# Kernel optimization log

Hardware: AMD Instinct MI355X
Metric: run time of the kernel (lower is better)

Reference implementation:

```python
import jax, jax.numpy as jnp
import numpy as np

B, CIN, COUT, H, W = 16, 64, 64, 128, 128
MH, MW = 32, 32  # retained Fourier modes


def setup_inputs() -> dict:
    key = jax.random.key(0)
    k1, k2, k3 = jax.random.split(key, 3)
    scale = 1.0 / (CIN * COUT)  # 'auto' scale in the torch module
    x = jax.random.normal(k1, (B, CIN, H, W), dtype=jnp.float32)
    # packed complex weight: dim0 = (real, imag), dim1 = corner (top=0, bottom=1)
    weight = scale * jax.random.normal(k2, (2, 2, CIN, COUT, MH, MW), dtype=jnp.float32)
    bias = scale * jax.random.normal(k3, (COUT, 1, 1), dtype=jnp.float32)
    return {"x": x, "weight": weight, "bias": bias, "super_res": 1}


def reference(x, weight, bias, super_res):
    b, ci, h, w = x.shape
    # rfft2 over the last two spatial dims (norm='backward' is default)
    xf = jnp.fft.rfft2(x.astype(jnp.float32), norm="backward")  # [b, ci, h, w//2+1] c64
    wc = (weight[0] + 1j * weight[1]).astype(jnp.complex64)  # [2, ci, co, mh, mw]
    # low-frequency corner contractions: bixy,ioxy->boxy
    top = jnp.einsum("bixy,ioxy->boxy", xf[:, :, :MH, :MW], wc[0])
    bot = jnp.einsum("bixy,ioxy->boxy", xf[:, :, h - MH:, :MW], wc[1])
    out_fft = jnp.zeros((b, COUT, h, w // 2 + 1), dtype=jnp.complex64)
    out_fft = out_fft.at[:, :, :MH, :MW:super_res].set(top)
    out_fft = out_fft.at[:, :, h - MH:, :MW:super_res].set(bot)
    out_size = (int(h * super_res), int(w * super_res))
    y = jnp.fft.irfft2(out_fft, s=out_size, norm="backward").astype(x.dtype)
    return y + bias  # bias [co,1,1] broadcasts over spatial dims
```

## Files before the change

kernel.cpp:

```cpp
#include <hip/hip_runtime.h>


__device__ __forceinline__ void build_tab(float* tabs) {
    int t = threadIdx.x;
    if (t < 128) {
        float ang = (float)t * 0.049087385212340517f;
        float s, c;
        sincosf(ang, &s, &c);
        tabs[t] = c;
        tabs[129 + t] = s;
    }
}

__global__ __launch_bounds__(256) void kAB(const float* __restrict__ x,
                                           float* __restrict__ XF) {
    __shared__ float tabs[258];
    __shared__ __align__(16) float smem[8704];
    build_tab(tabs);
    __syncthreads();
    int t = threadIdx.x;
    size_t bc = blockIdx.x;
    float* Twid = smem;
    float* xeo  = smem + 4096;
    #pragma unroll
    for (int i = 0; i < 16; ++i) {
        int e = t + i * 256;
        int w = e >> 6, q = e & 63, kx = q >> 1;
        int idx = (w * kx) & 127;
        Twid[e] = (q & 1) ? -tabs[129 + idx] : tabs[idx];
    }
    const float* xb = x + bc * 16384;
    int th = t & 31;
    int tq = t >> 5;
    int q0 = tq * 8;
    int wl4 = (t & 3) * 4;
    int hb  = t >> 2;
    float4 rlo0, rhi0, rlo1, rhi1;
    auto loadR = [&](int ph) {
        rlo0 = *(const float4*)(xb + hb * 128 + ph * 16 + wl4);
        rhi0 = *(const float4*)(xb + hb * 128 + ph * 16 + wl4 + 64);
        rlo1 = *(const float4*)(xb + (64 + hb) * 128 + ph * 16 + wl4);
        rhi1 = *(const float4*)(xb + (64 + hb) * 128 + ph * 16 + wl4 + 64);
    };
    auto writeR = [&]() {
        int h0 = hb, h1 = 64 + hb;
        *(float2*)(&xeo[(wl4+0)*260 + 2*h0]) = make_float2(rlo0.x+rhi0.x, rlo0.x-rhi0.x);
        *(float2*)(&xeo[(wl4+1)*260 + 2*h0]) = make_float2(rlo0.y+rhi0.y, rlo0.y-rhi0.y);
        *(float2*)(&xeo[(wl4+2)*260 + 2*h0]) = make_float2(rlo0.z+rhi0.z, rlo0.z-rhi0.z);
        *(float2*)(&xeo[(wl4+3)*260 + 2*h0]) = make_float2(rlo0.w+rhi0.w, rlo0.w-rhi0.w);
        *(float2*)(&xeo[(wl4+0)*260 + 2*h1]) = make_float2(rlo1.x+rhi1.x, rlo1.x-rhi1.x);
        *(float2*)(&xeo[(wl4+1)*260 + 2*h1]) = make_float2(rlo1.y+rhi1.y, rlo1.y-rhi1.y);
        *(float2*)(&xeo[(wl4+2)*260 + 2*h1]) = make_float2(rlo1.z+rhi1.z, rlo1.z-rhi1.z);
        *(float2*)(&xeo[(wl4+3)*260 + 2*h1]) = make_float2(rlo1.w+rhi1.w, rlo1.w-rhi1.w);
    };
    loadR(0);
    writeR();
    float4 acc[8];
    #pragma unroll
    for (int j = 0; j < 8; ++j) acc[j] = make_float4(0.f, 0.f, 0.f, 0.f);
    __syncthreads();
    for (int ph = 0; ph < 4; ++ph) {
        if (ph < 3) loadR(ph + 1);
        #pragma unroll 4
        for (int wl = 0; wl < 16; ++wl) {
            int w = ph * 16 + wl;
            const float* xr = &xeo[wl * 260 + 4 * th];
            float4 d0  = *(const float4*)(xr);
            float4 d1  = *(const float4*)(xr + 128);
            float4 tw0 = *(const float4*)(&Twid[w * 64 + q0]);
            float4 tw1 = *(const float4*)(&Twid[w * 64 + q0 + 4]);
            acc[0].x = fmaf(d0.x, tw0.x, acc[0].x); acc[0].y = fmaf(d0.x, tw0.y, acc[0].y);
            acc[0].z = fmaf(d0.y, tw0.z, acc[0].z); acc[0].w = fmaf(d0.y, tw0.w, acc[0].w);
            acc[1].x = fmaf(d0.x, tw1.x, acc[1].x); acc[1].y = fmaf(d0.x, tw1.y, acc[1].y);
            acc[1].z = fmaf(d0.y, tw1.z, acc[1].z); acc[1].w = fmaf(d0.y, tw1.w, acc[1].w);
            acc[2].x = fmaf(d0.z, tw0.x, acc[2].x); acc[2].y = fmaf(d0.z, tw0.y, acc[2].y);
            acc[2].z = fmaf(d0.w, tw0.z, acc[2].z); acc[2].w = fmaf(d0.w, tw0.w, acc[2].w);
            acc[3].x = fmaf(d0.z, tw1.x, acc[3].x); acc[3].y = fmaf(d0.z, tw1.y, acc[3].y);
            acc[3].z = fmaf(d0.w, tw1.z, acc[3].z); acc[3].w = fmaf(d0.w, tw1.w, acc[3].w);
            acc[4].x = fmaf(d1.x, tw0.x, acc[4].x); acc[4].y = fmaf(d1.x, tw0.y, acc[4].y);
            acc[4].z = fmaf(d1.y, tw0.z, acc[4].z); acc[4].w = fmaf(d1.y, tw0.w, acc[4].w);
            acc[5].x = fmaf(d1.x, tw1.x, acc[5].x); acc[5].y = fmaf(d1.x, tw1.y, acc[5].y);
            acc[5].z = fmaf(d1.y, tw1.z, acc[5].z); acc[5].w = fmaf(d1.y, tw1.w, acc[5].w);
            acc[6].x = fmaf(d1.z, tw0.x, acc[6].x); acc[6].y = fmaf(d1.z, tw0.y, acc[6].y);
            acc[6].z = fmaf(d1.w, tw0.z, acc[6].z); acc[6].w = fmaf(d1.w, tw0.w, acc[6].w);
            acc[7].x = fmaf(d1.z, tw1.x, acc[7].x); acc[7].y = fmaf(d1.z, tw1.y, acc[7].y);
            acc[7].z = fmaf(d1.w, tw1.z, acc[7].z); acc[7].w = fmaf(d1.w, tw1.w, acc[7].w);
        }
        __syncthreads();
        if (ph < 3) {
            writeR();
            __syncthreads();
        }
    }
    float* Af = smem;
    {
        int base = th * 68 + q0;
        *(float4*)(&Af[base])          = make_float4(acc[0].x+acc[4].x, acc[0].y+acc[4].y, acc[0].z+acc[4].z, acc[0].w+acc[4].w);
        *(float4*)(&Af[base + 4])      = make_float4(acc[1].x+acc[5].x, acc[1].y+acc[5].y, acc[1].z+acc[5].z, acc[1].w+acc[5].w);
        *(float4*)(&Af[2176 + base])   = make_float4(acc[0].x-acc[4].x, acc[0].y-acc[4].y, acc[0].z-acc[4].z, acc[0].w-acc[4].w);
        *(float4*)(&Af[2176 + base+4]) = make_float4(acc[1].x-acc[5].x, acc[1].y-acc[5].y, acc[1].z-acc[5].z, acc[1].w-acc[5].w);
        *(float4*)(&Af[4352 + base])   = make_float4(acc[2].x+acc[6].x, acc[2].y+acc[6].y, acc[2].z+acc[6].z, acc[2].w+acc[6].w);
        *(float4*)(&Af[4352 + base+4]) = make_float4(acc[3].x+acc[7].x, acc[3].y+acc[7].y, acc[3].z+acc[7].z, acc[3].w+acc[7].w);
        *(float4*)(&Af[6528 + base])   = make_float4(acc[2].x-acc[6].x, acc[2].y-acc[6].y, acc[2].z-acc[6].z, acc[2].w-acc[6].w);
        *(float4*)(&Af[6528 + base+4]) = make_float4(acc[3].x-acc[7].x, acc[3].y-acc[7].y, acc[3].z-acc[7].z, acc[3].w-acc[7].w);
    }
    __syncthreads();
    {
        int k = t & 31, kxg = t >> 5;
        int kx0 = kxg * 4;
        int sig = k & 1;
        const float* pe = Af + sig * 2176;
        const float* po = Af + 4352 + sig * 2176;
        int a2 = (2 * k) & 127;
        float ca = tabs[a2], sa = tabs[129 + a2];
        float ce = 1.f, se = 0.f;
        float co_ = tabs[k], so_ = tabs[129 + k];
        float4 P1 = {0,0,0,0}, P2 = {0,0,0,0}, P3 = {0,0,0,0}, P4 = {0,0,0,0};
        for (int m = 0; m < 32; ++m) {
            float4 ae01 = *(const float4*)(pe + m * 68 + 2 * kx0);
            float4 ae23 = *(const float4*)(pe + m * 68 + 2 * kx0 + 4);
            float4 ao01 = *(const float4*)(po + m * 68 + 2 * kx0);
            float4 ao23 = *(const float4*)(po + m * 68 + 2 * kx0 + 4);
            P1.x = fmaf(ae01.x, ce, P1.x); P1.x = fmaf(ao01.x, co_, P1.x);
            P2.x = fmaf(ae01.y, se, P2.x); P2.x = fmaf(ao01.y, so_, P2.x);
            P3.x = fmaf(ae01.y, ce, P3.x); P3.x = fmaf(ao01.y, co_, P3.x);
            P4.x = fmaf(ae01.x, se, P4.x); P4.x = fmaf(ao01.x, so_, P4.x);
            P1.y = fmaf(ae01.z, ce, P1.y); P1.y = fmaf(ao01.z, co_, P1.y);
            P2.y = fmaf(ae01.w, se, P2.y); P2.y = fmaf(ao01.w, so_, P2.y);
            P3.y = fmaf(ae01.w, ce, P3.y); P3.y = fmaf(ao01.w, co_, P3.y);
            P4.y = fmaf(ae01.z, se, P4.y); P4.y = fmaf(ao01.z, so_, P4.y);
            P1.z = fmaf(ae23.x, ce, P1.z); P1.z = fmaf(ao23.x, co_, P1.z);
            P2.z = fmaf(ae23.y, se, P2.z); P2.z = fmaf(ao23.y, so_, P2.z);
            P3.z = fmaf(ae23.y, ce, P3.z); P3.z = fmaf(ao23.y, co_, P3.z);
            P4.z = fmaf(ae23.x, se, P4.z); P4.z = fmaf(ao23.x, so_, P4.z);
            P1.w = fmaf(ae23.z, ce, P1.w); P1.w = fmaf(ao23.z, co_, P1.w);
            P2.w = fmaf(ae23.w, se, P2.w); P2.w = fmaf(ao23.w, so_, P2.w);
            P3.w = fmaf(ae23.w, ce, P3.w); P3.w = fmaf(ao23.w, co_, P3.w);
            P4.w = fmaf(ae23.z, se, P4.w); P4.w = fmaf(ao23.z, so_, P4.w);
            float t1 = se * sa, t2 = ce * sa;
            float cen = fmaf(ce, ca, -t1);
            float sen = fmaf(se, ca, t2);
            ce = cen; se = sen;
            float t3 = so_ * sa, t4 = co_ * sa;
            float con = fmaf(co_, ca, -t3);
            float son = fmaf(so_, ca, t4);
            co_ = con; so_ = son;
        }
        float* xfb = XF + bc * 4096;
        *(float4*)(xfb + (k * 32 + kx0) * 2) =
            make_float4(P1.x + P2.x, P3.x - P4.x, P1.y + P2.y, P3.y - P4.y);
        *(float4*)(xfb + (k * 32 + kx0) * 2 + 4) =
            make_float4(P1.z + P2.z, P3.z - P4.z, P1.w + P2.w, P3.w - P4.w);
        if (k) {
            *(float4*)(xfb + ((64 - k) * 32 + kx0) * 2) =
                make_float4(P1.x - P2.x, P3.x + P4.x, P1.y - P2.y, P3.y + P4.y);
            *(float4*)(xfb + ((64 - k) * 32 + kx0) * 2 + 4) =
                make_float4(P1.z - P2.z, P3.z + P4.z, P1.w - P2.w, P3.w + P4.w);
        }
        if (t < 32) {
            int kx = t;
            float re = 0.f, im = 0.f;
            #pragma unroll 8
            for (int m = 0; m < 32; ++m) {
                float2 aep = *(const float2*)(&Af[       m * 68 + 2 * kx]);
                float2 aop = *(const float2*)(&Af[4352 + m * 68 + 2 * kx]);
                float sg = (m & 1) ? -1.f : 1.f;
                re = fmaf(sg, aep.x - aop.y, re);
                im = fmaf(sg, aep.y + aop.x, im);
            }
            xfb[(32 * 32 + kx) * 2]     = re;
            xfb[(32 * 32 + kx) * 2 + 1] = im;
        }
    }
}

__global__ __launch_bounds__(256, 4) void kC(const float* __restrict__ XF,
                                             const float* __restrict__ Wgt,
                                             float* __restrict__ YF0,
                                             float* __restrict__ YF1) {
    __shared__ float2 Xs[2048];
    int t = threadIdx.x;
    int bid = blockIdx.x;
    int cih = bid & 1;
    int mxh = (bid >> 1) & 1;
    int cot = (bid >> 2) & 3;
    int my  = (bid >> 4) & 31;
    int c   = bid >> 9;
    int co0 = cot * 16;
    int slotbase = (c * 32 + my) * 32 + mxh * 16;
    int mx = t & 15;
    int co_l = t >> 4;
    int co = co0 + co_l;
    int ci0 = cih * 32;
    float2 acc[16];
    #pragma unroll
    for (int i = 0; i < 16; ++i) acc[i] = make_float2(0.f, 0.f);
    const float* wp = Wgt + (size_t)c * 4194304 + (size_t)my * 32 + mxh * 16 + mx
                          + ((size_t)(ci0 * 64) + co) * 1024;
    float2 rw0[8], rw1[8], rw2[8], rw3[8], rx[8];
    auto loadW = [&](int cc, float2* rw) {
        #pragma unroll
        for (int j = 0; j < 8; ++j) {
            size_t off = (size_t)(cc * 8 + j) * 65536;
            rw[j].x = wp[off];
            rw[j].y = wp[off + 8388608];
        }
    };
    auto loadX = [&](int cc) {
        #pragma unroll
        for (int s = 0; s < 8; ++s) {
            int e = t + s * 256;
            int emx = e & 15, eb = (e >> 4) & 15, eci = e >> 8;
            int ci = ci0 + cc * 8 + eci;
            rx[s] = *(const float2*)(XF + ((size_t)(eb * 64 + ci) * 2048 + slotbase + emx) * 2);
        }
    };
    auto writeX = [&]() {
        #pragma unroll
        for (int s = 0; s < 8; ++s) Xs[t + s * 256] = rx[s];
    };
#define KC_COMPUTE(RW)                                                       \
    {                                                                        \
        _Pragma("unroll")                                                    \
        for (int j = 0; j < 8; ++j) {                                        \
            float2 w = RW[j];                                                \
            _Pragma("unroll")                                                \
            for (int b = 0; b < 16; ++b) {                                   \
                float2 xv = Xs[(j * 16 + b) * 16 + mx];                      \
                acc[b].x = fmaf(xv.x, w.x, acc[b].x);                        \
                acc[b].x = fmaf(-xv.y, w.y, acc[b].x);                       \
                acc[b].y = fmaf(xv.x, w.y, acc[b].y);                        \
                acc[b].y = fmaf(xv.y, w.x, acc[b].y);                        \
            }                                                                \
        }                                                                    \
    }
    loadX(0);
    loadW(0, rw0); loadW(1, rw1); loadW(2, rw2);
    writeX();
    __syncthreads();
    loadX(1);
    loadW(3, rw3);
    KC_COMPUTE(rw0);
    __syncthreads();
    writeX(); __syncthreads();
    loadX(2);
    KC_COMPUTE(rw1);
    __syncthreads();
    writeX(); __syncthreads();
    loadX(3);
    KC_COMPUTE(rw2);
    __syncthreads();
    writeX(); __syncthreads();
    KC_COMPUTE(rw3);
#undef KC_COMPUTE
    float* YF = cih ? YF1 : YF0;
    #pragma unroll
    for (int b = 0; b < 16; ++b) {
        *(float2*)(YF + ((size_t)(b * 64 + co) * 2048 + slotbase + mx) * 2) = acc[b];
    }
}

__global__ __launch_bounds__(256) void kDE(const float* __restrict__ YF0,
                                           const float* __restrict__ YF1,
                                           const float* __restrict__ bias,
                                           float* __restrict__ out) {
    __shared__ float tabs[258];
    __shared__ __align__(16) float Ts[8192];
    __shared__ __align__(16) float U[8448];
    build_tab(tabs);
    __syncthreads();
    int t = threadIdx.x;
    size_t bo = blockIdx.x;
    const float inv = 6.103515625e-05f;
    #pragma unroll
    for (int i = 0; i < 32; ++i) {
        int e = t + i * 256;
        int q = e >> 7, w = e & 127;
        int k = q >> 1;
        int idx = (k * w) & 127;
        float val;
        if (q == 0)      val = inv;
        else if (q == 1) val = 0.f;
        else if (q & 1)  val = -2.f * inv * tabs[129 + idx];
        else             val =  2.f * inv * tabs[idx];
        Ts[e] = val;
    }
    float* Qs = U;
    float* Rs = U + 2112;
    const float* y0 = YF0 + bo * 4096;
    const float* y1 = YF1 + bo * 4096;
    for (int u = t; u < 528; u += 256) {
        int k = u >> 4, kxf = (u & 15) * 4;
        float4 a0 = *(const float4*)(y0 + k * 64 + kxf);
        float4 a1 = *(const float4*)(y1 + k * 64 + kxf);
        float4 a = make_float4(a0.x+a1.x, a0.y+a1.y, a0.z+a1.z, a0.w+a1.w);
        float4 Q, R;
        if (k == 0) { Q = a; R = make_float4(0.f, 0.f, 0.f, 0.f); }
        else if (k == 32) { Q = a; R = make_float4(-a.x, -a.y, -a.z, -a.w); }
        else {
            float4 b0 = *(const float4*)(y0 + (64 - k) * 64 + kxf);
            float4 b1 = *(const float4*)(y1 + (64 - k) * 64 + kxf);
            float4 bb = make_float4(b0.x+b1.x, b0.y+b1.y, b0.z+b1.z, b0.w+b1.w);
            Q = make_float4(a.x+bb.x, a.y+bb.y, a.z+bb.z, a.w+bb.w);
            R = make_float4(a.x-bb.x, a.y-bb.y, a.z-bb.z, a.w-bb.w);
        }
        *(float4*)(&Qs[k * 64 + kxf]) = Q;
        *(float4*)(&Rs[k * 64 + kxf]) = R;
    }
    __syncthreads();
    int hh = t >> 2;
    int kx0 = (t & 3) * 8;
    float4 Ee0 = {0,0,0,0}, Ee1 = {0,0,0,0}, Ee2 = {0,0,0,0}, Ee3 = {0,0,0,0};
    float4 Eo0 = {0,0,0,0}, Eo1 = {0,0,0,0}, Eo2 = {0,0,0,0}, Eo3 = {0,0,0,0};
    int idx = 0;
#define KD_BODY(E0, E1, E2, E3, kk)                                          \
    {                                                                        \
        float c = tabs[idx], s = tabs[129 + idx];                            \
        const float4* Qp = (const float4*)(&Qs[(kk) * 64 + kx0 * 2]);        \
        const float4* Rp = (const float4*)(&Rs[(kk) * 64 + kx0 * 2]);        \
        float4 Qv, Rv;                                                       \
        Qv = Qp[0]; Rv = Rp[0];                                              \
        E0.x = fmaf(c, Qv.x, E0.x); E0.x = fmaf(-s, Rv.y, E0.x);             \
        E0.y = fmaf(c, Qv.y, E0.y); E0.y = fmaf(s, Rv.x, E0.y);              \
        E0.z = fmaf(c, Qv.z, E0.z); E0.z = fmaf(-s, Rv.w, E0.z);             \
        E0.w = fmaf(c, Qv.w, E0.w); E0.w = fmaf(s, Rv.z, E0.w);              \
        Qv = Qp[1]; Rv = Rp[1];                                              \
        E1.x = fmaf(c, Qv.x, E1.x); E1.x = fmaf(-s, Rv.y, E1.x);             \
        E1.y = fmaf(c, Qv.y, E1.y); E1.y = fmaf(s, Rv.x, E1.y);              \
        E1.z = fmaf(c, Qv.z, E1.z); E1.z = fmaf(-s, Rv.w, E1.z);             \
        E1.w = fmaf(c, Qv.w, E1.w); E1.w = fmaf(s, Rv.z, E1.w);              \
        Qv = Qp[2]; Rv = Rp[2];                                              \
        E2.x = fmaf(c, Qv.x, E2.x); E2.x = fmaf(-s, Rv.y, E2.x);             \
        E2.y = fmaf(c, Qv.y, E2.y); E2.y = fmaf(s, Rv.x, E2.y);              \
        E2.z = fmaf(c, Qv.z, E2.z); E2.z = fmaf(-s, Rv.w, E2.z);             \
        E2.w = fmaf(c, Qv.w, E2.w); E2.w = fmaf(s, Rv.z, E2.w);              \
        Qv = Qp[3]; Rv = Rp[3];                                              \
        E3.x = fmaf(c, Qv.x, E3.x); E3.x = fmaf(-s, Rv.y, E3.x);             \
        E3.y = fmaf(c, Qv.y, E3.y); E3.y = fmaf(s, Rv.x, E3.y);              \
        E3.z = fmaf(c, Qv.z, E3.z); E3.z = fmaf(-s, Rv.w, E3.z);             \
        E3.w = fmaf(c, Qv.w, E3.w); E3.w = fmaf(s, Rv.z, E3.w);              \
        idx = (idx + hh) & 127;                                              \
    }
    for (int u = 0; u < 16; ++u) {
        KD_BODY(Ee0, Ee1, Ee2, Ee3, 2 * u);
        KD_BODY(Eo0, Eo1, Eo2, Eo3, 2 * u + 1);
    }
    KD_BODY(Ee0, Ee1, Ee2, Ee3, 32);
#undef KD_BODY
    __syncthreads();
    float* Zt = U;
    {
        float* zr = &Zt[(2 * kx0) * 132 + hh];
        float* zs = zr + 64;
        zr[0*132]  = Ee0.x + Eo0.x;  zs[0*132]  = Ee0.x - Eo0.x;
        zr[1*132]  = Ee0.y + Eo0.y;  zs[1*132]  = Ee0.y - Eo0.y;
        zr[2*132]  = Ee0.z + Eo0.z;  zs[2*132]  = Ee0.z - Eo0.z;
        zr[3*132]  = Ee0.w + Eo0.w;  zs[3*132]  = Ee0.w - Eo0.w;
        zr[4*132]  = Ee1.x + Eo1.x;  zs[4*132]  = Ee1.x - Eo1.x;
        zr[5*132]  = Ee1.y + Eo1.y;  zs[5*132]  = Ee1.y - Eo1.y;
        zr[6*132]  = Ee1.z + Eo1.z;  zs[6*132]  = Ee1.z - Eo1.z;
        zr[7*132]  = Ee1.w + Eo1.w;  zs[7*132]  = Ee1.w - Eo1.w;
        zr[8*132]  = Ee2.x + Eo2.x;  zs[8*132]  = Ee2.x - Eo2.x;
        zr[9*132]  = Ee2.y + Eo2.y;  zs[9*132]  = Ee2.y - Eo2.y;
        zr[10*132] = Ee2.z + Eo2.z;  zs[10*132] = Ee2.z - Eo2.z;
        zr[11*132] = Ee2.w + Eo2.w;  zs[11*132] = Ee2.w - Eo2.w;
        zr[12*132] = Ee3.x + Eo3.x;  zs[12*132] = Ee3.x - Eo3.x;
        zr[13*132] = Ee3.y + Eo3.y;  zs[13*132] = Ee3.y - Eo3.y;
        zr[14*132] = Ee3.z + Eo3.z;  zs[14*132] = Ee3.z - Eo3.z;
        zr[15*132] = Ee3.w + Eo3.w;  zs[15*132] = Ee3.w - Eo3.w;
    }
    __syncthreads();
    int w0 = (t & 31) * 4;
    int h0 = (t >> 5) * 16;
    float4 a0 = {0,0,0,0}, a1 = {0,0,0,0}, a2 = {0,0,0,0}, a3 = {0,0,0,0};
    float4 a4 = {0,0,0,0}, a5 = {0,0,0,0}, a6 = {0,0,0,0}, a7 = {0,0,0,0};
    float4 a8 = {0,0,0,0}, a9 = {0,0,0,0}, a10 = {0,0,0,0}, a11 = {0,0,0,0};
    float4 a12 = {0,0,0,0}, a13 = {0,0,0,0}, a14 = {0,0,0,0}, a15 = {0,0,0,0};
#define KE_ROW(A, ZV) A.x = fmaf(ZV, tw.x, A.x); A.y = fmaf(ZV, tw.y, A.y); \
                      A.z = fmaf(ZV, tw.z, A.z); A.w = fmaf(ZV, tw.w, A.w);
    #pragma unroll 2
    for (int q = 0; q < 64; ++q) {
        const float4* zp = (const float4*)(&Zt[q * 132 + h0]);
        float4 za = zp[0], zb = zp[1], zc = zp[2], zd = zp[3];
        float4 tw = *(const float4*)(&Ts[q * 128 + w0]);
        KE_ROW(a0, za.x)  KE_ROW(a1, za.y)  KE_ROW(a2, za.z)  KE_ROW(a3, za.w)
        KE_ROW(a4, zb.x)  KE_ROW(a5, zb.y)  KE_ROW(a6, zb.z)  KE_ROW(a7, zb.w)
        KE_ROW(a8, zc.x)  KE_ROW(a9, zc.y)  KE_ROW(a10, zc.z) KE_ROW(a11, zc.w)
        KE_ROW(a12, zd.x) KE_ROW(a13, zd.y) KE_ROW(a14, zd.z) KE_ROW(a15, zd.w)
    }
#undef KE_ROW
    float bv = bias[(int)(bo & 63)];
    float* ob = out + ((size_t)(bo * 128 + h0)) * 128 + w0;
#define KE_ST(J, A) { float4 r = A; r.x += bv; r.y += bv; r.z += bv; r.w += bv; \
                      *(float4*)(ob + (size_t)(J) * 128) = r; }
    KE_ST(0, a0)   KE_ST(1, a1)   KE_ST(2, a2)   KE_ST(3, a3)
    KE_ST(4, a4)   KE_ST(5, a5)   KE_ST(6, a6)   KE_ST(7, a7)
    KE_ST(8, a8)   KE_ST(9, a9)   KE_ST(10, a10) KE_ST(11, a11)
    KE_ST(12, a12) KE_ST(13, a13) KE_ST(14, a14) KE_ST(15, a15)
#undef KE_ST
}

extern "C" void kernel_launch(void* const* d_in, const int* in_sizes, int n_in,
                              void* d_out, int out_size, void* d_ws, size_t ws_size,
                              hipStream_t stream) {
    (void)in_sizes; (void)n_in; (void)out_size; (void)ws_size;
    const float* x    = (const float*)d_in[0];
    const float* wgt  = (const float*)d_in[1];
    const float* bias = (const float*)d_in[2];
    float* outp   = (float*)d_out;
    char* ws = (char*)d_ws;
    float* bufXF  = (float*)(ws + (48u << 20));
    float* bufYF0 = (float*)(ws);
    float* bufYF1 = (float*)(ws + (16u << 20));
    hipLaunchKernelGGL(kAB, dim3(1024), dim3(256), 0, stream, x, bufXF);
    hipLaunchKernelGGL(kC, dim3(1024), dim3(256), 0, stream, bufXF, wgt, bufYF0, bufYF1);
    hipLaunchKernelGGL(kDE, dim3(1024), dim3(256), 0, stream, bufYF0, bufYF1, bias, outp);
}
```

Measured before the change: 123.3 us.

## Exploit even/odd frequency symmetry to halve final inverse DFT twiddle work

The last stage of the inverse transform along W now computes only 64 output columns per row. Even and odd frequency terms are accumulated separately, and the two halves of the output come from their sum and difference, using the fact that the twiddle for w+64 changes sign only on odd k. This halves the twiddle table and roughly halves the FMA count and twiddle LDS reads in kDE's main loop. In exchange each thread holds 64 float accumulators and writes float2 stores instead of float4, which may raise register pressure.

```diff
diff --git a/kernel.cpp b/kernel.cpp
--- a/kernel.cpp
+++ b/kernel.cpp
@@ -265,7 +265,7 @@
                                            const float* __restrict__ bias,
                                            float* __restrict__ out) {
     __shared__ float tabs[258];
-    __shared__ __align__(16) float Ts[8192];
+    __shared__ __align__(16) float Ts[4096];
     __shared__ __align__(16) float U[8448];
     build_tab(tabs);
     __syncthreads();
@@ -273,9 +273,9 @@
     size_t bo = blockIdx.x;
     const float inv = 6.103515625e-05f;
     #pragma unroll
-    for (int i = 0; i < 32; ++i) {
+    for (int i = 0; i < 16; ++i) {
         int e = t + i * 256;
-        int q = e >> 7, w = e & 127;
+        int q = e >> 6, w = e & 63;
         int k = q >> 1;
         int idx = (k * w) & 127;
         float val;
@@ -370,34 +370,67 @@
         zr[15*132] = Ee3.w + Eo3.w;  zs[15*132] = Ee3.w - Eo3.w;
     }
     __syncthreads();
-    int w0 = (t & 31) * 4;
+    int w0 = (t & 31) * 2;
     int h0 = (t >> 5) * 16;
-    float4 a0 = {0,0,0,0}, a1 = {0,0,0,0}, a2 = {0,0,0,0}, a3 = {0,0,0,0};
-    float4 a4 = {0,0,0,0}, a5 = {0,0,0,0}, a6 = {0,0,0,0}, a7 = {0,0,0,0};
-    float4 a8 = {0,0,0,0}, a9 = {0,0,0,0}, a10 = {0,0,0,0}, a11 = {0,0,0,0};
-    float4 a12 = {0,0,0,0}, a13 = {0,0,0,0}, a14 = {0,0,0,0}, a15 = {0,0,0,0};
-#define KE_ROW(A, ZV) A.x = fmaf(ZV, tw.x, A.x); A.y = fmaf(ZV, tw.y, A.y); \
-                      A.z = fmaf(ZV, tw.z, A.z); A.w = fmaf(ZV, tw.w, A.w);
+    float2 We[16], Wo[16];
+    #pragma unroll
+    for (int j = 0; j < 16; ++j) { We[j] = make_float2(0.f, 0.f); Wo[j] = make_float2(0.f, 0.f); }
+#define KE_K(E, K)                                                            \
+    {                                                                         \
+        const float4* zpe = (const float4*)(&Zt[(2*(K)) * 132 + h0]);         \
+        const float4* zpo = (const float4*)(&Zt[(2*(K)+1) * 132 + h0]);       \
+        float2 twe = *(const float2*)(&Ts[(2*(K)) * 64 + w0]);                \
+        float2 two = *(const float2*)(&Ts[(2*(K)+1) * 64 + w0]);              \
+        float4 e0 = zpe[0], e1 = zpe[1], e2 = zpe[2], e3 = zpe[3];            \
+        float4 o0 = zpo[0], o1 = zpo[1], o2 = zpo[2], o3 = zpo[3];            \
+        E[0].x  = fmaf(e0.x, twe.x, E[0].x);  E[0].x  = fmaf(o0.x, two.x, E[0].x);   \
+        E[0].y  = fmaf(e0.x, twe.y, E[0].y);  E[0].y  = fmaf(o0.x, two.y, E[0].y);   \
+        E[1].x  = fmaf(e0.y, twe.x, E[1].x);  E[1].x  = fmaf(o0.y, two.x, E[1].x);   \
+        E[1].y  = fmaf(e0.y, twe.y, E[1].y);  E[1].y  = fmaf(o0.y, two.y, E[1].y);   \
+        E[2].x  = fmaf(e0.z, twe.x, E[2].x);  E[2].x  = fmaf(o0.z, two.x, E[2].x);   \
+        E[2].y  = fmaf(e0.z, twe.y, E[2].y);  E[2].y  = fmaf(o0.z, two.y, E[2].y);   \
+        E[3].x  = fmaf(e0.w, twe.x, E[3].x);  E[3].x  = fmaf(o0.w, two.x, E[3].x);   \
+        E[3].y  = fmaf(e0.w, twe.y, E[3].y);  E[3].y  = fmaf(o0.w, two.y, E[3].y);   \
+        E[4].x  = fmaf(e1.x, twe.x, E[4].x);  E[4].x  = fmaf(o1.x, two.x, E[4].x);   \
+        E[4].y  = fmaf(e1.x, twe.y, E[4].y);  E[4].y  = fmaf(o1.x, two.y, E[4].y);   \
+        E[5].x  = fmaf(e1.y, twe.x, E[5].x);  E[5].x  = fmaf(o1.y, two.x, E[5].x);   \
+        E[5].y  = fmaf(e1.y, twe.y, E[5].y);  E[5].y  = fmaf(o1.y, two.y, E[5].y);   \
+        E[6].x  = fmaf(e1.z, twe.x, E[6].x);  E[6].x  = fmaf(o1.z, two.x, E[6].x);   \
+        E[6].y  = fmaf(e1.z, twe.y, E[6].y);  E[6].y  = fmaf(o1.z, two.y, E[6].y);   \
+        E[7].x  = fmaf(e1.w, twe.x, E[7].x);  E[7].x  = fmaf(o1.w, two.x, E[7].x);   \
+        E[7].y  = fmaf(e1.w, twe.y, E[7].y);  E[7].y  = fmaf(o1.w, two.y, E[7].y);   \
+        E[8].x  = fmaf(e2.x, twe.x, E[8].x);  E[8].x  = fmaf(o2.x, two.x, E[8].x);   \
+        E[8].y  = fmaf(e2.x, twe.y, E[8].y);  E[8].y  = fmaf(o2.x, two.y, E[8].y);   \
+        E[9].x  = fmaf(e2.y, twe.x, E[9].x);  E[9].x  = fmaf(o2.y, two.x, E[9].x);   \
+        E[9].y  = fmaf(e2.y, twe.y, E[9].y);  E[9].y  = fmaf(o2.y, two.y, E[9].y);   \
+        E[10].x = fmaf(e2.z, twe.x, E[10].x); E[10].x = fmaf(o2.z, two.x, E[10].x);  \
+        E[10].y = fmaf(e2.z, twe.y, E[10].y); E[10].y = fmaf(o2.z, two.y, E[10].y);  \
+        E[11].x = fmaf(e2.w, twe.x, E[11].x); E[11].x = fmaf(o2.w, two.x, E[11].x);  \
+        E[11].y = fmaf(e2.w, twe.y, E[11].y); E[11].y = fmaf(o2.w, two.y, E[11].y);  \
+        E[12].x = fmaf(e3.x, twe.x, E[12].x); E[12].x = fmaf(o3.x, two.x, E[12].x);  \
+        E[12].y = fmaf(e3.x, twe.y, E[12].y); E[12].y = fmaf(o3.x, two.y, E[12].y);  \
+        E[13].x = fmaf(e3.y, twe.x, E[13].x); E[13].x = fmaf(o3.y, two.x, E[13].x);  \
+        E[13].y = fmaf(e3.y, twe.y, E[13].y); E[13].y = fmaf(o3.y, two.y, E[13].y);  \
+        E[14].x = fmaf(e3.z, twe.x, E[14].x); E[14].x = fmaf(o3.z, two.x, E[14].x);  \
+        E[14].y = fmaf(e3.z, twe.y, E[14].y); E[14].y = fmaf(o3.z, two.y, E[14].y);  \
+        E[15].x = fmaf(e3.w, twe.x, E[15].x); E[15].x = fmaf(o3.w, two.x, E[15].x);  \
+        E[15].y = fmaf(e3.w, twe.y, E[15].y); E[15].y = fmaf(o3.w, two.y, E[15].y);  \
+    }
     #pragma unroll 2
-    for (int q = 0; q < 64; ++q) {
-        const float4* zp = (const float4*)(&Zt[q * 132 + h0]);
-        float4 za = zp[0], zb = zp[1], zc = zp[2], zd = zp[3];
-        float4 tw = *(const float4*)(&Ts[q * 128 + w0]);
-        KE_ROW(a0, za.x)  KE_ROW(a1, za.y)  KE_ROW(a2, za.z)  KE_ROW(a3, za.w)
-        KE_ROW(a4, zb.x)  KE_ROW(a5, zb.y)  KE_ROW(a6, zb.z)  KE_ROW(a7, zb.w)
-        KE_ROW(a8, zc.x)  KE_ROW(a9, zc.y)  KE_ROW(a10, zc.z) KE_ROW(a11, zc.w)
-        KE_ROW(a12, zd.x) KE_ROW(a13, zd.y) KE_ROW(a14, zd.z) KE_ROW(a15, zd.w)
-    }
-#undef KE_ROW
+    for (int u = 0; u < 16; ++u) {
+        KE_K(We, 2 * u);
+        KE_K(Wo, 2 * u + 1);
+    }
+#undef KE_K
     float bv = bias[(int)(bo & 63)];
-    float* ob = out + ((size_t)(bo * 128 + h0)) * 128 + w0;
-#define KE_ST(J, A) { float4 r = A; r.x += bv; r.y += bv; r.z += bv; r.w += bv; \
-                      *(float4*)(ob + (size_t)(J) * 128) = r; }
-    KE_ST(0, a0)   KE_ST(1, a1)   KE_ST(2, a2)   KE_ST(3, a3)
-    KE_ST(4, a4)   KE_ST(5, a5)   KE_ST(6, a6)   KE_ST(7, a7)
-    KE_ST(8, a8)   KE_ST(9, a9)   KE_ST(10, a10) KE_ST(11, a11)
-    KE_ST(12, a12) KE_ST(13, a13) KE_ST(14, a14) KE_ST(15, a15)
-#undef KE_ST
+    float* ob = out + ((size_t)(bo * 128 + h0)) * 128;
+    #pragma unroll
+    for (int j = 0; j < 16; ++j) {
+        float2 lo = make_float2(We[j].x + Wo[j].x + bv, We[j].y + Wo[j].y + bv);
+        float2 hi = make_float2(We[j].x - Wo[j].x + bv, We[j].y - Wo[j].y + bv);
+        *(float2*)(ob + (size_t)j * 128 + w0)      = lo;
+        *(float2*)(ob + (size_t)j * 128 + w0 + 64) = hi;
+    }
 }
 
 extern "C" void kernel_launch(void* const* d_in, const int* in_sizes, int n_in,
```

After: 116.9 us. -5.2%, faster.
